# Kernel tuning notes

Measured on AMD Instinct MI355X. Metric: run time of the kernel, lower is better.

The kernel has to match this reference:

```python
import jax, jax.numpy as jnp
import numpy as np

IN_C, OUT_C, NUM_VARS = 8, 8, 3
MODES1, MODES2 = 16, 16
TDIM = 256
B, H, W = 16, 256, 256
SCALE = 1.0 / (IN_C * OUT_C)


def setup_inputs() -> dict:
    key = jax.random.key(0)
    k1, k2, k3, k4, k5, k6 = jax.random.split(key, 6)
    wshape = (IN_C, OUT_C, NUM_VARS, MODES1, MODES2, TDIM)
    return {
        "t": jax.random.uniform(k1, (B, TDIM), dtype=jnp.float32),
        "x": jax.random.normal(k2, (B, IN_C, NUM_VARS, H, W), dtype=jnp.float32),
        "w1r": SCALE * jax.random.uniform(k3, wshape, dtype=jnp.float32),
        "w1i": SCALE * jax.random.uniform(k4, wshape, dtype=jnp.float32),
        "w2r": SCALE * jax.random.uniform(k5, wshape, dtype=jnp.float32),
        "w2i": SCALE * jax.random.uniform(k6, wshape, dtype=jnp.float32),
    }


def reference(t, x, w1r, w1i, w2r, w2i):
    m1, m2 = MODES1, MODES2
    b, _, v, h, w = x.shape
    wf = w // 2 + 1
    w1 = (w1r + 1j * w1i).astype(jnp.complex64)
    w2 = (w2r + 1j * w2i).astype(jnp.complex64)
    tc = t.astype(jnp.complex64)

    # FFT over last two spatial axes: [b, i, v, h, wf]
    x_ft = jnp.fft.rfft2(x)

    # time-conditioned spectral weights: [b, i, o, v, m1, m2]
    tw1 = jnp.einsum("bt,iovxyt->biovxy", tc, w1)
    tw2 = jnp.einsum("bt,iovxyt->biovxy", tc, w2)

    # complex spectral mixing on the retained low/high modes
    top = jnp.einsum("bivxy,biovxy->bovxy", x_ft[:, :, :, :m1, :m2], tw1)
    bot = jnp.einsum("bivxy,biovxy->bovxy", x_ft[:, :, :, -m1:, :m2], tw2)

    out_ft = jnp.zeros((b, OUT_C, v, h, wf), dtype=jnp.complex64)
    out_ft = out_ft.at[:, :, :, :m1, :m2].set(top)
    out_ft = out_ft.at[:, :, :, -m1:, :m2].set(bot)

    return jnp.fft.irfft2(out_ft, s=(h, w))
```

## Files before the change

### kernel.cpp

```cpp
#include <hip/hip_runtime.h>

#define BB 16
#define IC 8
#define OC 8
#define NV 3
#define M1 16
#define M2 16
#define HH 256
#define WW 256
#define NIMG_IN  (BB*IC*NV)
#define NIMG_OUT (BB*OC*NV)
#define NROWS    (IC*OC*NV*M1*M2)
#define TWO_PI 6.28318530717958647692f

#define STEPJ(J, E, XV)                                   \
  ar##J.x = fmaf((E).x, (XV).x, ar##J.x);                 \
  ar##J.y = fmaf((E).x, (XV).y, ar##J.y);                 \
  ai##J.x = fmaf(-(E).y, (XV).x, ai##J.x);                \
  ai##J.y = fmaf(-(E).y, (XV).y, ai##J.y);

#define ROW(XV, H) {                                      \
  int m_ = (kbase * (H)) & 255;                           \
  float2 e_;                                              \
  e_ = tbl[m_]; STEPJ(0, e_, XV) m_ = (m_ + (H)) & 255;   \
  e_ = tbl[m_]; STEPJ(1, e_, XV) m_ = (m_ + (H)) & 255;   \
  e_ = tbl[m_]; STEPJ(2, e_, XV) m_ = (m_ + (H)) & 255;   \
  e_ = tbl[m_]; STEPJ(3, e_, XV) m_ = (m_ + (H)) & 255;   \
  e_ = tbl[m_]; STEPJ(4, e_, XV) m_ = (m_ + (H)) & 255;   \
  e_ = tbl[m_]; STEPJ(5, e_, XV) m_ = (m_ + (H)) & 255;   \
  e_ = tbl[m_]; STEPJ(6, e_, XV) m_ = (m_ + (H)) & 255;   \
  e_ = tbl[m_]; STEPJ(7, e_, XV) m_ = (m_ + (H)) & 255;   \
  e_ = tbl[m_]; STEPJ(8, e_, XV)                          \
}

#define STORJ(J) p[(J)*4+0]=ar##J.x; p[(J)*4+1]=ar##J.y; p[(J)*4+2]=ai##J.x; p[(J)*4+3]=ai##J.y;
#define LOADJ(J) ar##J.x+=p[(J)*4+0]; ar##J.y+=p[(J)*4+1]; ai##J.x+=p[(J)*4+2]; ai##J.y+=p[(J)*4+3];
#define OUTJ(J)  yo4[(kbase+(J))*128 + col2] = make_float4(ar##J.x, ai##J.x, ar##J.y, ai##J.y);

__global__ __launch_bounds__(256, 3) void k1a_rowdft(const float* __restrict__ x,
                                                     float2* __restrict__ y) {
  __shared__ float2 tbl[256];
  __shared__ float red[128][37];
  const int tid = threadIdx.x;
  const int bid = blockIdx.x;
  const int half = (bid >= 384) ? 1 : 0;
  const int img = bid - half * 384;
  const int kbase = half ? 9 : 0;
  const int kcount = half ? 8 : 9;
  {
    float s, c;
    sincosf((float)tid * (TWO_PI / 256.0f), &s, &c);
    tbl[tid] = make_float2(c, s);
  }
  __syncthreads();

  const int col2 = tid & 127;
  const int hq = tid >> 7;
  const int hbase = hq * 128;
  const float2* xp = (const float2*)(x + (size_t)img * 65536) + col2;

  float2 ar0 = {0,0}, ar1 = {0,0}, ar2 = {0,0}, ar3 = {0,0}, ar4 = {0,0},
         ar5 = {0,0}, ar6 = {0,0}, ar7 = {0,0}, ar8 = {0,0};
  float2 ai0 = {0,0}, ai1 = {0,0}, ai2 = {0,0}, ai3 = {0,0}, ai4 = {0,0},
         ai5 = {0,0}, ai6 = {0,0}, ai7 = {0,0}, ai8 = {0,0};

  float2 c0 = xp[(size_t)(hbase + 0) * 128];
  float2 c1 = xp[(size_t)(hbase + 1) * 128];
  float2 c2 = xp[(size_t)(hbase + 2) * 128];
  float2 c3 = xp[(size_t)(hbase + 3) * 128];

  for (int hi = 0; hi < 128; hi += 4) {
    const int hn = (hbase + hi + 4) & 255;
    float2 n0 = xp[(size_t)(hn + 0) * 128];
    float2 n1 = xp[(size_t)(hn + 1) * 128];
    float2 n2 = xp[(size_t)(hn + 2) * 128];
    float2 n3 = xp[(size_t)(hn + 3) * 128];

    const int h = hbase + hi;
    ROW(c0, h + 0)
    ROW(c1, h + 1)
    ROW(c2, h + 2)
    ROW(c3, h + 3)

    c0 = n0; c1 = n1; c2 = n2; c3 = n3;
  }

  if (hq) {
    float* p = &red[col2][0];
    STORJ(0) STORJ(1) STORJ(2) STORJ(3) STORJ(4) STORJ(5) STORJ(6) STORJ(7) STORJ(8)
  }
  __syncthreads();
  if (!hq) {
    const float* p = &red[col2][0];
    LOADJ(0) LOADJ(1) LOADJ(2) LOADJ(3) LOADJ(4) LOADJ(5) LOADJ(6) LOADJ(7) LOADJ(8)
    float4* yo4 = (float4*)(y + (size_t)img * 4352);
    OUTJ(0) OUTJ(1) OUTJ(2) OUTJ(3) OUTJ(4) OUTJ(5) OUTJ(6) OUTJ(7)
    if (kcount == 9) { OUTJ(8) }
  }
}

__global__ __launch_bounds__(256) void k1b_coldft(const float2* __restrict__ y,
                                                  float2* __restrict__ Xf) {
  __shared__ float2 tbl[256];
  __shared__ float2 yb[17 * 257];
  const int tid = threadIdx.x;
  const int img = blockIdx.x;
  {
    float s, c;
    sincosf((float)tid * (TWO_PI / 256.0f), &s, &c);
    tbl[tid] = make_float2(c, s);
  }
  const float2* yg = y + (size_t)img * 4352;
  for (int n = tid; n < 4352; n += 256) {
    int kx = n >> 8, w = n & 255;
    yb[kx * 257 + w] = yg[n];
  }
  __syncthreads();

  float2* XfImg = Xf + (size_t)img * 512;
  for (int n = tid; n < 512; n += 256) {
    int row = n >> 4, ky = n & 15;
    int kxl = (row < 16) ? row : (32 - row);
    float sgn = (row < 16) ? 1.0f : -1.0f;
    float Xr = 0.0f, Xi = 0.0f;
    int m = 0;
    for (int w2 = 0; w2 < 256; w2++) {
      float2 yv = yb[kxl * 257 + w2];
      float2 e = tbl[m];
      m = (m + ky) & 255;
      float yy = yv.y * sgn;
      Xr += yv.x * e.x + yy * e.y;
      Xi += yy * e.x - yv.x * e.y;
    }
    XfImg[n] = make_float2(Xr, Xi);
  }
}

__global__ __launch_bounds__(256) void k2_tw(const float* __restrict__ t,
                                             const float* __restrict__ w1r,
                                             const float* __restrict__ w1i,
                                             const float* __restrict__ w2r,
                                             const float* __restrict__ w2i,
                                             float2* __restrict__ tw1,
                                             float2* __restrict__ tw2) {
  __shared__ float tL[16 * 260];
  __shared__ float4 wA[2][16 * 64];
  const int tid = threadIdx.x;
  const int row0 = blockIdx.x * 16;
  const int b = tid >> 4;
  const int r = tid & 15;
  const int c = r & 7;

  {
    const float4* tg = (const float4*)t;
    float4* ts = (float4*)tL;
    for (int n = tid; n < 1024; n += 256) ts[(n >> 6) * 65 + (n & 63)] = tg[n];
  }

  float o1r, o1i, o2r, o2i;
  const float4* tb4 = (const float4*)tL + b * 65;

  for (int pass = 0; pass < 2; pass++) {
    const float* wa = pass ? w2r : w1r;
    const float* wb = pass ? w2i : w1i;
    const float4* ga = (const float4*)(wa + (size_t)row0 * 256);
    const float4* gb = (const float4*)(wb + (size_t)row0 * 256);
    for (int n = tid; n < 1024; n += 256) {
      int rr = n >> 6, t4 = n & 63;
      int sidx = (rr << 6) | (t4 ^ (rr & 7));
      wA[0][sidx] = ga[n];
      wA[1][sidx] = gb[n];
    }
    __syncthreads();

    const float4* ra4 = wA[0] + (r << 6);
    const float4* rb4 = wA[1] + (r << 6);
    float arr = 0.0f, aii = 0.0f;
#pragma unroll 8
    for (int t4 = 0; t4 < 64; t4++) {
      float4 tv = tb4[t4];
      int s = t4 ^ c;
      float4 va = ra4[s];
      float4 vb = rb4[s];
      arr += tv.x * va.x + tv.y * va.y + tv.z * va.z + tv.w * va.w;
      aii += tv.x * vb.x + tv.y * vb.y + tv.z * vb.z + tv.w * vb.w;
    }
    if (pass) { o2r = arr; o2i = aii; } else { o1r = arr; o1i = aii; }
    __syncthreads();
  }

  tw1[(size_t)b * NROWS + row0 + r] = make_float2(o1r, o1i);
  tw2[(size_t)b * NROWS + row0 + r] = make_float2(o2r, o2i);
}

__global__ __launch_bounds__(256) void k3_mix(const float2* __restrict__ Xf,
                                              const float2* __restrict__ tw1,
                                              const float2* __restrict__ tw2,
                                              float2* __restrict__ ftT,
                                              float2* __restrict__ ftB) {
  const int n = blockIdx.x * 256 + threadIdx.x;
  const int xy = n & 255;
  const int ov = n >> 8;
  const int v = ov % 3;
  const int o = (ov / 3) & 7;
  const int b = n / (OC * NV * 256);

  float tr = 0.0f, ti2 = 0.0f, br = 0.0f, bi = 0.0f;
#pragma unroll
  for (int i = 0; i < IC; i++) {
    const float2 xt = Xf[(size_t)(((b * IC + i) * NV + v) << 9) + xy];
    const float2 xb = Xf[(size_t)(((b * IC + i) * NV + v) << 9) + 256 + xy];
    const int r = ((i * OC + o) * NV + v) * 256 + xy;
    float2 u1 = tw1[(size_t)b * NROWS + r];
    float2 u2 = tw2[(size_t)b * NROWS + r];
    tr += xt.x * u1.x - xt.y * u1.y;
    ti2 += xt.x * u1.y + xt.y * u1.x;
    br += xb.x * u2.x - xb.y * u2.y;
    bi += xb.x * u2.y + xb.y * u2.x;
  }
  const int nout = ((b * OC + o) * NV + v) * 256 + xy;
  ftT[nout] = make_float2(tr, ti2);
  ftB[nout] = make_float2(br, bi);
}

__global__ __launch_bounds__(256) void k4a_hdft(const float2* __restrict__ ftT,
                                                const float2* __restrict__ ftB,
                                                float2* __restrict__ G) {
  __shared__ float2 tbl[256];
  __shared__ float2 ftL[512];
  const int tid = threadIdx.x;
  const int img = blockIdx.x;
  {
    float s, c;
    sincosf((float)tid * (TWO_PI / 256.0f), &s, &c);
    tbl[tid] = make_float2(c, s);
    ftL[tid] = ftT[(size_t)img * 256 + tid];
    ftL[256 + tid] = ftB[(size_t)img * 256 + tid];
  }
  __syncthreads();

  const int h = tid;
  float gr[16], gi[16];
#pragma unroll
  for (int ky = 0; ky < 16; ky++) { gr[ky] = 0.0f; gi[ky] = 0.0f; }
  for (int row = 0; row < 32; row++) {
    int kxv = (row < 16) ? row : (224 + row);
    float2 e = tbl[(kxv * h) & 255];
#pragma unroll
    for (int ky = 0; ky < 16; ky++) {
      float2 f = ftL[row * 16 + ky];
      gr[ky] += f.x * e.x - f.y * e.y;
      gi[ky] += f.x * e.y + f.y * e.x;
    }
  }
  float2* Gi = G + (size_t)img * 4096;
#pragma unroll
  for (int ky = 0; ky < 16; ky++) Gi[ky * 256 + h] = make_float2(gr[ky], gi[ky]);
}

__global__ __launch_bounds__(256) void k4b_wdft(const float2* __restrict__ G,
                                                float* __restrict__ out) {
  __shared__ float2 tbl[256];
  __shared__ float2 PL[16 * 256];
  __shared__ float2 gt[512];
  const int tid = threadIdx.x;
  const int img = blockIdx.x >> 3;
  const int h0 = (blockIdx.x & 7) * 32;
  {
    float s, c;
    sincosf((float)tid * (TWO_PI / 256.0f), &s, &c);
    tbl[tid] = make_float2(c, s);
  }
  __syncthreads();
  for (int n = tid; n < 4096; n += 256) {
    int ky = n >> 8, w = n & 255;
    float2 e = tbl[(ky * w) & 255];
    float sc = (ky == 0) ? (1.0f / 65536.0f) : (2.0f / 65536.0f);
    PL[n] = make_float2(e.x * sc, e.y * sc);
  }
  const float2* Gi = G + (size_t)img * 4096;
  for (int n = tid; n < 512; n += 256) {
    int ky = n >> 5, hh = n & 31;
    gt[n] = Gi[ky * 256 + h0 + hh];
  }
  __syncthreads();

  const int w0 = tid & 63;
  const int hq = tid >> 6;
  float acc[8][4];
#pragma unroll
  for (int a = 0; a < 8; a++)
#pragma unroll
    for (int j = 0; j < 4; j++) acc[a][j] = 0.0f;

#pragma unroll 4
  for (int ky = 0; ky < 16; ky++) {
    float2 p0 = PL[ky * 256 + w0];
    float2 p1 = PL[ky * 256 + w0 + 64];
    float2 p2 = PL[ky * 256 + w0 + 128];
    float2 p3 = PL[ky * 256 + w0 + 192];
#pragma unroll
    for (int a = 0; a < 8; a++) {
      float2 g = gt[ky * 32 + hq * 8 + a];
      acc[a][0] += g.x * p0.x - g.y * p0.y;
      acc[a][1] += g.x * p1.x - g.y * p1.y;
      acc[a][2] += g.x * p2.x - g.y * p2.y;
      acc[a][3] += g.x * p3.x - g.y * p3.y;
    }
  }
  float* obase = out + (size_t)img * 65536 + (size_t)(h0 + hq * 8) * 256;
#pragma unroll
  for (int a = 0; a < 8; a++) {
#pragma unroll
    for (int j = 0; j < 4; j++) obase[a * 256 + w0 + 64 * j] = acc[a][j];
  }
}

extern "C" void kernel_launch(void* const* d_in, const int* in_sizes, int n_in,
                              void* d_out, int out_size, void* d_ws, size_t ws_size,
                              hipStream_t stream) {
  const float* t = (const float*)d_in[0];
  const float* x = (const float*)d_in[1];
  const float* w1r = (const float*)d_in[2];
  const float* w1i = (const float*)d_in[3];
  const float* w2r = (const float*)d_in[4];
  const float* w2i = (const float*)d_in[5];
  float* out = (float*)d_out;

  float2* R1 = (float2*)d_ws;
  float2* y = R1;
  float2* tw1 = R1;
  float2* tw2 = R1 + 786432;
  float2* G = R1;
  float2* Xf = R1 + 1671168;
  float2* ftT = Xf + 196608;
  float2* ftB = ftT + 98304;

  k1a_rowdft<<<NIMG_IN * 2, 256, 0, stream>>>(x, y);
  k1b_coldft<<<NIMG_IN, 256, 0, stream>>>(y, Xf);
  k2_tw<<<NROWS / 16, 256, 0, stream>>>(t, w1r, w1i, w2r, w2i, tw1, tw2);
  k3_mix<<<(BB * OC * NV * 256) / 256, 256, 0, stream>>>(Xf, tw1, tw2, ftT, ftB);
  k4a_hdft<<<NIMG_OUT, 256, 0, stream>>>(ftT, ftB, G);
  k4b_wdft<<<NIMG_OUT * 8, 256, 0, stream>>>(G, out);
}
```

Baseline: 426.8 us.

## Restructure time-weight contraction to one row per thread with register prefetch

The t·W contraction kernel now gives each thread one full weight row and accumulates all 16 batches and both weight sets in registers. It reads t from a transposed shared-memory copy as broadcast float4 values. It streams the four weight tensors straight from global memory with a two-window register double buffer, replacing the shared-memory staging and the two sequential passes. The aim is to drop the LDS traffic and barriers and reuse each weight value across all batches. In exchange, each lane's loads are strided by a row, so coalescing is poorer, and with 64-thread blocks only a few waves run per CU to hide latency.

```diff
diff --git a/kernel.cpp b/kernel.cpp
--- a/kernel.cpp
+++ b/kernel.cpp
@@ -136,61 +136,96 @@
   }
 }
 
-__global__ __launch_bounds__(256) void k2_tw(const float* __restrict__ t,
-                                             const float* __restrict__ w1r,
-                                             const float* __restrict__ w1i,
-                                             const float* __restrict__ w2r,
-                                             const float* __restrict__ w2i,
-                                             float2* __restrict__ tw1,
-                                             float2* __restrict__ tw2) {
-  __shared__ float tL[16 * 260];
-  __shared__ float4 wA[2][16 * 64];
-  const int tid = threadIdx.x;
-  const int row0 = blockIdx.x * 16;
-  const int b = tid >> 4;
-  const int r = tid & 15;
-  const int c = r & 7;
+#define COMP(v, c) ((c) == 0 ? (v).x : (c) == 1 ? (v).y : (c) == 2 ? (v).z : (v).w)
+
+#define FMAB(B, TV)                                  \
+  acc[B].x = fmaf((TV), w1rv, acc[B].x);             \
+  acc[B].y = fmaf((TV), w1iv, acc[B].y);             \
+  acc[B].z = fmaf((TV), w2rv, acc[B].z);             \
+  acc[B].w = fmaf((TV), w2iv, acc[B].w);
+
+__global__ __launch_bounds__(64, 1) void k2_tw(const float* __restrict__ t,
+                                               const float* __restrict__ w1r,
+                                               const float* __restrict__ w1i,
+                                               const float* __restrict__ w2r,
+                                               const float* __restrict__ w2i,
+                                               float2* __restrict__ tw1,
+                                               float2* __restrict__ tw2) {
+  __shared__ float tT[256 * 16];
+  const int tid = threadIdx.x;
 
   {
     const float4* tg = (const float4*)t;
-    float4* ts = (float4*)tL;
-    for (int n = tid; n < 1024; n += 256) ts[(n >> 6) * 65 + (n & 63)] = tg[n];
-  }
-
-  float o1r, o1i, o2r, o2i;
-  const float4* tb4 = (const float4*)tL + b * 65;
-
-  for (int pass = 0; pass < 2; pass++) {
-    const float* wa = pass ? w2r : w1r;
-    const float* wb = pass ? w2i : w1i;
-    const float4* ga = (const float4*)(wa + (size_t)row0 * 256);
-    const float4* gb = (const float4*)(wb + (size_t)row0 * 256);
-    for (int n = tid; n < 1024; n += 256) {
-      int rr = n >> 6, t4 = n & 63;
-      int sidx = (rr << 6) | (t4 ^ (rr & 7));
-      wA[0][sidx] = ga[n];
-      wA[1][sidx] = gb[n];
-    }
-    __syncthreads();
-
-    const float4* ra4 = wA[0] + (r << 6);
-    const float4* rb4 = wA[1] + (r << 6);
-    float arr = 0.0f, aii = 0.0f;
-#pragma unroll 8
-    for (int t4 = 0; t4 < 64; t4++) {
-      float4 tv = tb4[t4];
-      int s = t4 ^ c;
-      float4 va = ra4[s];
-      float4 vb = rb4[s];
-      arr += tv.x * va.x + tv.y * va.y + tv.z * va.z + tv.w * va.w;
-      aii += tv.x * vb.x + tv.y * vb.y + tv.z * vb.z + tv.w * vb.w;
-    }
-    if (pass) { o2r = arr; o2i = aii; } else { o1r = arr; o1i = aii; }
-    __syncthreads();
-  }
-
-  tw1[(size_t)b * NROWS + row0 + r] = make_float2(o1r, o1i);
-  tw2[(size_t)b * NROWS + row0 + r] = make_float2(o2r, o2i);
+#pragma unroll
+    for (int i = 0; i < 16; i++) {
+      int n = (tid << 4) + i;
+      float4 v = tg[n];
+      int b = n >> 6;
+      int k0 = (n & 63) << 2;
+      tT[(k0 + 0) * 16 + b] = v.x;
+      tT[(k0 + 1) * 16 + b] = v.y;
+      tT[(k0 + 2) * 16 + b] = v.z;
+      tT[(k0 + 3) * 16 + b] = v.w;
+    }
+  }
+  __syncthreads();
+
+  const int row = blockIdx.x * 64 + tid;
+  const float4* p1r = (const float4*)w1r + (size_t)row * 64;
+  const float4* p1i = (const float4*)w1i + (size_t)row * 64;
+  const float4* p2r = (const float4*)w2r + (size_t)row * 64;
+  const float4* p2i = (const float4*)w2i + (size_t)row * 64;
+
+  float4 acc[16];
+#pragma unroll
+  for (int b = 0; b < 16; b++) acc[b] = make_float4(0.f, 0.f, 0.f, 0.f);
+
+  float4 cur[16], nxt[16];
+#pragma unroll
+  for (int j = 0; j < 4; j++) {
+    cur[j] = p1r[j]; cur[4 + j] = p1i[j]; cur[8 + j] = p2r[j]; cur[12 + j] = p2i[j];
+  }
+#pragma unroll
+  for (int j = 0; j < 4; j++) {
+    nxt[j] = p1r[4 + j]; nxt[4 + j] = p1i[4 + j]; nxt[8 + j] = p2r[4 + j]; nxt[12 + j] = p2i[4 + j];
+  }
+
+  for (int win = 0; win < 16; win++) {
+#pragma unroll
+    for (int kk = 0; kk < 16; kk++) {
+      const int k = (win << 4) + kk;
+      const float* tp = tT + k * 16;
+      float4 tq[4];
+      tq[0] = *(const float4*)(tp);
+      tq[1] = *(const float4*)(tp + 4);
+      tq[2] = *(const float4*)(tp + 8);
+      tq[3] = *(const float4*)(tp + 12);
+      const float w1rv = COMP(cur[(kk >> 2)], kk & 3);
+      const float w1iv = COMP(cur[4 + (kk >> 2)], kk & 3);
+      const float w2rv = COMP(cur[8 + (kk >> 2)], kk & 3);
+      const float w2iv = COMP(cur[12 + (kk >> 2)], kk & 3);
+      FMAB(0, tq[0].x)  FMAB(1, tq[0].y)  FMAB(2, tq[0].z)  FMAB(3, tq[0].w)
+      FMAB(4, tq[1].x)  FMAB(5, tq[1].y)  FMAB(6, tq[1].z)  FMAB(7, tq[1].w)
+      FMAB(8, tq[2].x)  FMAB(9, tq[2].y)  FMAB(10, tq[2].z) FMAB(11, tq[2].w)
+      FMAB(12, tq[3].x) FMAB(13, tq[3].y) FMAB(14, tq[3].z) FMAB(15, tq[3].w)
+    }
+#pragma unroll
+    for (int j = 0; j < 16; j++) cur[j] = nxt[j];
+    const int wn = (win + 2 < 16) ? (win + 2) : 15;
+#pragma unroll
+    for (int j = 0; j < 4; j++) {
+      nxt[j]      = p1r[wn * 4 + j];
+      nxt[4 + j]  = p1i[wn * 4 + j];
+      nxt[8 + j]  = p2r[wn * 4 + j];
+      nxt[12 + j] = p2i[wn * 4 + j];
+    }
+  }
+
+#pragma unroll
+  for (int b = 0; b < 16; b++) {
+    tw1[(size_t)b * NROWS + row] = make_float2(acc[b].x, acc[b].y);
+    tw2[(size_t)b * NROWS + row] = make_float2(acc[b].z, acc[b].w);
+  }
 }
 
 __global__ __launch_bounds__(256) void k3_mix(const float2* __restrict__ Xf,
@@ -338,7 +373,7 @@
 
   k1a_rowdft<<<NIMG_IN * 2, 256, 0, stream>>>(x, y);
   k1b_coldft<<<NIMG_IN, 256, 0, stream>>>(y, Xf);
-  k2_tw<<<NROWS / 16, 256, 0, stream>>>(t, w1r, w1i, w2r, w2i, tw1, tw2);
+  k2_tw<<<NROWS / 64, 64, 0, stream>>>(t, w1r, w1i, w2r, w2i, tw1, tw2);
   k3_mix<<<(BB * OC * NV * 256) / 256, 256, 0, stream>>>(Xf, tw1, tw2, ftT, ftB);
   k4a_hdft<<<NIMG_OUT, 256, 0, stream>>>(ftT, ftB, G);
   k4b_wdft<<<NIMG_OUT * 8, 256, 0, stream>>>(G, out);
```

After: 494.0 us. 15.7% more time.
